# Performance work log

Hardware: AMD Instinct MI355X
Metric: run time of the kernel (lower is better)

The kernel has to match this reference:

```python
import jax, jax.numpy as jnp
import numpy as np

M = 30000      # total nodes
D = 64         # hidden_channels
B = 256        # number of graphs
E = 480000     # number of edges
NUM_ITER = 3   # Newton-Schulz iterations
EPS_TRIU = 0.001  # fix_triu diagonal jitter


def setup_inputs() -> dict:
    key = jax.random.key(0)
    k1, k2, k3 = jax.random.split(key, 3)
    x = jax.random.normal(k1, (M, D), dtype=jnp.float32)
    # sorted segment ids, every graph non-empty (sorted_randint semantics)
    batch = ((jnp.arange(M) * B) // M).astype(jnp.int32)
    edge = jax.random.randint(k2, (2, E), 0, M)
    W_att = jax.random.normal(k3, (D * D, 1), dtype=jnp.float32) / D
    b_att = jnp.zeros((1,), dtype=jnp.float32)
    return {"x": x, "batch": batch, "edge": edge, "W_att": W_att, "b_att": b_att}


def _segment_softmax(v, seg, num_segments):
    # v: [M], seg: [M] -> per-segment softmax
    m = jax.ops.segment_max(v, seg, num_segments=num_segments)
    e = jnp.exp(v - m[seg])
    s = jax.ops.segment_sum(e, seg, num_segments=num_segments)
    return e / s[seg]


def _sqrtm_ns(A, n_iter):
    # Newton-Schulz iterative matrix square root (MPN-COV Sqrtm)
    d = A.shape[-1]
    I = jnp.eye(d, dtype=A.dtype)
    normA = jnp.trace(A, axis1=-2, axis2=-1)[:, None, None]  # [B,1,1]
    Y = A / normA
    Z = jnp.broadcast_to(I, A.shape)
    for _ in range(n_iter):
        T = 0.5 * (3.0 * I - jnp.matmul(Z, Y))
        Y = jnp.matmul(Y, T)
        Z = jnp.matmul(T, Z)
    return Y * jnp.sqrt(normA)


def reference(x, batch, edge, W_att, b_att):
    Mn, Dd = x.shape
    # per-node outer products: einsum 'ik,kj->kij' on (x^T, x)
    wj = x[:, :, None] * x[:, None, :]              # [M, D, D]
    flat = wj.reshape(Mn, Dd * Dd)                  # [M, D*D]
    imp = (flat @ W_att + b_att)[:, 0]              # [M]
    imp = _segment_softmax(imp, batch, B)[:, None]  # scatter_softmax
    # scatter_mean(imp * flat, batch)
    num = jax.ops.segment_sum(imp * flat, batch, num_segments=B)
    cnt = jax.ops.segment_sum(jnp.ones((Mn,), x.dtype), batch, num_segments=B)
    out = (num / jnp.maximum(cnt, 1.0)[:, None]).reshape(B, Dd, Dd)
    # fix_triu: add eps * I before matrix sqrt
    out = out + EPS_TRIU * jnp.eye(Dd, dtype=out.dtype)
    out = _sqrtm_ns(out, NUM_ITER)
    # Triuvec: upper triangle incl. diagonal
    iu, ju = jnp.triu_indices(Dd)
    out = out[:, iu, ju]                            # [B, D*(D+1)/2]
    return out.reshape(B, -1)
```

## Files before the change

### kernel.cpp

```cpp
#include <hip/hip_runtime.h>
#include <math.h>

#define MN       30000
#define BSEG     256
#define EPS_TRIU 0.001f

#define XR_H 0
#define XR_L 8192
#define XT_H 16384
#define XT_L 24576
#define WT_H 32768
#define WT_L 36864
#define P_H 0
#define P_L 4096
#define Q_H 8192
#define Q_L 12288
#define R_H 16384
#define R_L 20480
#define S_H 24576
#define S_L 28672
#define V_H 32768
#define V_L 36864
#define IMP_F 20480
#define SWG_F 20608
#define SCL_F 20736
#define LDS_F4 5185

typedef __attribute__((ext_vector_type(8))) short bf16x8;
typedef __attribute__((ext_vector_type(4))) float f32x4;
#define MFMA_BF16(a, b, c) __builtin_amdgcn_mfma_f32_16x16x32_bf16(a, b, c, 0, 0, 0)

__device__ __forceinline__ short f2bf(float f) {
  unsigned u = __float_as_uint(f);
  u += 0x7FFF + ((u >> 16) & 1);
  return (short)(u >> 16);
}
__device__ __forceinline__ float bf2f(short s) {
  return __uint_as_float(((unsigned)(unsigned short)s) << 16);
}
__device__ __forceinline__ int sw64(int r, int c) { return (r << 6) + (c ^ ((r & 7) << 3)); }
__device__ __forceinline__ int sw128(int r, int c) { return (r << 7) + (c ^ ((r & 15) << 3)); }

template <int EPIT>
__device__ __forceinline__ void mm8(unsigned short* U, int dh, int dl,
                                    int ah_, int al_, int bh_, int bl_,
                                    int w, int r16, int kq) {
  const int mb = w >> 1;
  const int nb0 = (w & 1) << 1;
  const int ra = (mb << 4) + r16;
  const int mB = (mb << 4) + (kq << 2);
  bf16x8 Ah[2], Al[2];
#pragma unroll
  for (int ks = 0; ks < 2; ++ks) {
    const int ia = sw64(ra, (ks << 5) + (kq << 3));
    Ah[ks] = *(const bf16x8*)(U + ah_ + ia);
    Al[ks] = *(const bf16x8*)(U + al_ + ia);
  }
#pragma unroll
  for (int h = 0; h < 2; ++h) {
    const int nr = ((nb0 + h) << 4) + r16;
    bf16x8 Bh[2], Bl[2];
#pragma unroll
    for (int ks = 0; ks < 2; ++ks) {
      const int ib = sw64(nr, (ks << 5) + (kq << 3));
      Bh[ks] = *(const bf16x8*)(U + bh_ + ib);
      Bl[ks] = *(const bf16x8*)(U + bl_ + ib);
    }
    f32x4 acc = (f32x4)0.0f;
#pragma unroll
    for (int ks = 0; ks < 2; ++ks) {
      acc = MFMA_BF16(Ah[ks], Bh[ks], acc);
      acc = MFMA_BF16(Ah[ks], Bl[ks], acc);
      acc = MFMA_BF16(Al[ks], Bh[ks], acc);
    }
    short4 h4, l4;
#pragma unroll
    for (int e = 0; e < 4; ++e) {
      float v = acc[e];
      if (EPIT) v = -0.5f * v + ((mB + e) == nr ? 1.5f : 0.0f);
      const short hh = f2bf(v);
      ((short*)&h4)[e] = hh;
      ((short*)&l4)[e] = f2bf(v - bf2f(hh));
    }
    const int id = sw64(nr, mB);
    *(short4*)(U + dh + id) = h4;
    *(short4*)(U + dl + id) = l4;
  }
}

__device__ __forceinline__ void mm8_y3(unsigned short* U, int ah_, int al_,
                                       int bh_, int bl_, int w, float scale,
                                       float* __restrict__ ob, int r16, int kq) {
  const int mb = w >> 1;
  const int nb0 = (w & 1) << 1;
  if (mb > nb0 + 1) return;
  const int ra = (mb << 4) + r16;
  const int mB = (mb << 4) + (kq << 2);
  bf16x8 Ah[2], Al[2];
#pragma unroll
  for (int ks = 0; ks < 2; ++ks) {
    const int ia = sw64(ra, (ks << 5) + (kq << 3));
    Ah[ks] = *(const bf16x8*)(U + ah_ + ia);
    Al[ks] = *(const bf16x8*)(U + al_ + ia);
  }
#pragma unroll
  for (int h = 0; h < 2; ++h) {
    const int nb = nb0 + h;
    if (mb > nb) continue;
    const int nr = (nb << 4) + r16;
    bf16x8 Bh[2], Bl[2];
#pragma unroll
    for (int ks = 0; ks < 2; ++ks) {
      const int ib = sw64(nr, (ks << 5) + (kq << 3));
      Bh[ks] = *(const bf16x8*)(U + bh_ + ib);
      Bl[ks] = *(const bf16x8*)(U + bl_ + ib);
    }
    f32x4 acc = (f32x4)0.0f;
#pragma unroll
    for (int ks = 0; ks < 2; ++ks) {
      acc = MFMA_BF16(Ah[ks], Bh[ks], acc);
      acc = MFMA_BF16(Ah[ks], Bl[ks], acc);
      acc = MFMA_BF16(Al[ks], Bh[ks], acc);
    }
#pragma unroll
    for (int e = 0; e < 4; ++e) {
      const int m = mB + e;
      if (m <= nr) ob[((m * (129 - m)) >> 1) + nr - m] = acc[e] * scale;
    }
  }
}

template <int EPIT>
__device__ __forceinline__ void mm4(unsigned short* U, int dh, int dl,
                                    int ah_, int al_, int bh_, int bl_,
                                    int mq, int nq, int r16, int kq) {
  bf16x8 Ah[2][2], Al[2][2], Bh[2][2], Bl[2][2];
#pragma unroll
  for (int blk = 0; blk < 2; ++blk) {
    const int ra = (mq << 5) + (blk << 4) + r16;
    const int rb = (nq << 5) + (blk << 4) + r16;
#pragma unroll
    for (int ks = 0; ks < 2; ++ks) {
      const int co = (ks << 5) + (kq << 3);
      const int ia = sw64(ra, co), ib = sw64(rb, co);
      Ah[blk][ks] = *(const bf16x8*)(U + ah_ + ia);
      Al[blk][ks] = *(const bf16x8*)(U + al_ + ia);
      Bh[blk][ks] = *(const bf16x8*)(U + bh_ + ib);
      Bl[blk][ks] = *(const bf16x8*)(U + bl_ + ib);
    }
  }
#pragma unroll
  for (int mb = 0; mb < 2; ++mb)
#pragma unroll
    for (int nb = 0; nb < 2; ++nb) {
      f32x4 acc = (f32x4)0.0f;
#pragma unroll
      for (int ks = 0; ks < 2; ++ks) {
        acc = MFMA_BF16(Ah[mb][ks], Bh[nb][ks], acc);
        acc = MFMA_BF16(Ah[mb][ks], Bl[nb][ks], acc);
        acc = MFMA_BF16(Al[mb][ks], Bh[nb][ks], acc);
      }
      const int nr = (nq << 5) + (nb << 4) + r16;
      const int mB = (mq << 5) + (mb << 4) + (kq << 2);
      short4 h4, l4;
#pragma unroll
      for (int e = 0; e < 4; ++e) {
        float v = acc[e];
        if (EPIT) v = -0.5f * v + ((mB + e) == nr ? 1.5f : 0.0f);
        const short hh = f2bf(v);
        ((short*)&h4)[e] = hh;
        ((short*)&l4)[e] = f2bf(v - bf2f(hh));
      }
      const int id = sw64(nr, mB);
      *(short4*)(U + dh + id) = h4;
      *(short4*)(U + dl + id) = l4;
    }
}

extern "C" __global__ __launch_bounds__(512, 1) void readout_fused(
    const float* __restrict__ x, const float* __restrict__ Watt, float* __restrict__ out) {
  __shared__ float4 lds4[LDS_F4];
  float* ldsf = (float*)lds4;
  unsigned short* U = (unsigned short*)lds4;

  const int b = blockIdx.x;
  const int t = threadIdx.x;
  const int w = t >> 6, lane = t & 63;
  const int r16 = lane & 15, kq = lane >> 4;
  const int start = (b * MN + BSEG - 1) / BSEG;
  const int end = ((b + 1) * MN + BSEG - 1) / BSEG;
  const int n = end - start;

  const float4* W4 = (const float4*)Watt;
  const float4* X4 = (const float4*)x;

  if (t < 128) ldsf[IMP_F + t] = 0.0f;
  if (t == 128) ldsf[SCL_F] = 0.0f;
  const bool doW = (t < 256);
  const int kt = t >> 4, nt = t & 15;
  float4 gw[4];
  if (doW) {
#pragma unroll
    for (int i = 0; i < 4; ++i) gw[i] = W4[((kt << 2) + i) * 16 + nt];
  }
  {
    const int jt = t >> 4, dt = t & 15;
    const int j4 = jt << 2, d4 = dt << 2;
    float4 g[4];
#pragma unroll
    for (int i = 0; i < 4; ++i)
      g[i] = (j4 + i < n) ? X4[(size_t)(start + j4 + i) * 16 + dt]
                          : make_float4(0.f, 0.f, 0.f, 0.f);
    short hs[4][4], ls[4][4];
#pragma unroll
    for (int i = 0; i < 4; ++i)
#pragma unroll
      for (int e = 0; e < 4; ++e) {
        const float val = (&g[i].x)[e];
        const short hh = f2bf(val);
        hs[i][e] = hh;
        ls[i][e] = f2bf(val - bf2f(hh));
      }
#pragma unroll
    for (int i = 0; i < 4; ++i) {
      short4 h4, l4;
#pragma unroll
      for (int e = 0; e < 4; ++e) { ((short*)&h4)[e] = hs[i][e]; ((short*)&l4)[e] = ls[i][e]; }
      const int ir = sw64(j4 + i, d4);
      *(short4*)(U + XR_H + ir) = h4;
      *(short4*)(U + XR_L + ir) = l4;
    }
#pragma unroll
    for (int e = 0; e < 4; ++e) {
      short4 h4, l4;
#pragma unroll
      for (int i = 0; i < 4; ++i) { ((short*)&h4)[i] = hs[i][e]; ((short*)&l4)[i] = ls[i][e]; }
      const int it = sw128(d4 + e, j4);
      *(short4*)(U + XT_H + it) = h4;
      *(short4*)(U + XT_L + it) = l4;
    }
  }
  if (doW) {
    const int k4 = kt << 2, n4 = nt << 2;
#pragma unroll
    for (int e = 0; e < 4; ++e) {
      short4 h4, l4;
#pragma unroll
      for (int i = 0; i < 4; ++i) {
        const float val = (&gw[i].x)[e];
        const short hh = f2bf(val);
        ((short*)&h4)[i] = hh;
        ((short*)&l4)[i] = f2bf(val - bf2f(hh));
      }
      const int idx = sw64(n4 + e, k4);
      *(short4*)(U + WT_H + idx) = h4;
      *(short4*)(U + WT_L + idx) = l4;
    }
  }
  __syncthreads();

  {
    const int mq2 = w >> 1, nq2 = w & 1;
    bf16x8 Ah[2][2], Al[2][2];
#pragma unroll
    for (int mb = 0; mb < 2; ++mb) {
      const int ra = (mq2 << 5) + (mb << 4) + r16;
#pragma unroll
      for (int ks = 0; ks < 2; ++ks) {
        const int ia = sw64(ra, (ks << 5) + (kq << 3));
        Ah[mb][ks] = *(const bf16x8*)(U + XR_H + ia);
        Al[mb][ks] = *(const bf16x8*)(U + XR_L + ia);
      }
    }
    float c[2][4] = {};
#pragma unroll
    for (int nb = 0; nb < 2; ++nb) {
      const int rb = ((nq2 << 1) + nb) * 16 + r16;
      bf16x8 Bh[2], Bl[2];
#pragma unroll
      for (int ks = 0; ks < 2; ++ks) {
        const int ib = sw64(rb, (ks << 5) + (kq << 3));
        Bh[ks] = *(const bf16x8*)(U + WT_H + ib);
        Bl[ks] = *(const bf16x8*)(U + WT_L + ib);
      }
#pragma unroll
      for (int mb = 0; mb < 2; ++mb) {
        f32x4 acc = (f32x4)0.0f;
#pragma unroll
        for (int ks = 0; ks < 2; ++ks) {
          acc = MFMA_BF16(Ah[mb][ks], Bh[ks], acc);
          acc = MFMA_BF16(Ah[mb][ks], Bl[ks], acc);
          acc = MFMA_BF16(Al[mb][ks], Bh[ks], acc);
        }
        const int mBase = (mq2 << 5) + (mb << 4) + (kq << 2);
        const int xi = sw128(rb, mBase);
        short4 xh = *(const short4*)(U + XT_H + xi);
        short4 xl = *(const short4*)(U + XT_L + xi);
#pragma unroll
        for (int e = 0; e < 4; ++e)
          c[mb][e] += acc[e] * (bf2f(((short*)&xh)[e]) + bf2f(((short*)&xl)[e]));
      }
    }
#pragma unroll
    for (int s = 1; s <= 8; s <<= 1)
#pragma unroll
      for (int mb = 0; mb < 2; ++mb)
#pragma unroll
        for (int e = 0; e < 4; ++e) c[mb][e] += __shfl_xor(c[mb][e], s, 64);
    if (r16 == 0)
#pragma unroll
      for (int mb = 0; mb < 2; ++mb)
#pragma unroll
        for (int e = 0; e < 4; ++e)
          atomicAdd(&ldsf[IMP_F + (mq2 << 5) + (mb << 4) + (kq << 2) + e], c[mb][e]);
  }
  __syncthreads();

  bf16x8 pxh0 = *(const bf16x8*)(U + XT_H + t * 8);
  bf16x8 pxl0 = *(const bf16x8*)(U + XT_L + t * 8);
  bf16x8 pxh1 = *(const bf16x8*)(U + XT_H + (t + 512) * 8);
  bf16x8 pxl1 = *(const bf16x8*)(U + XT_L + (t + 512) * 8);
  if (t < 64) {
    float v0 = (t < n) ? ldsf[IMP_F + t] : -3.0e38f;
    float v1 = (t + 64 < n) ? ldsf[IMP_F + t + 64] : -3.0e38f;
    float m = fmaxf(v0, v1);
#pragma unroll
    for (int s = 32; s; s >>= 1) m = fmaxf(m, __shfl_xor(m, s, 64));
    float e0 = (t < n) ? expf(v0 - m) : 0.0f;
    float e1 = (t + 64 < n) ? expf(v1 - m) : 0.0f;
    float se = e0 + e1;
#pragma unroll
    for (int s = 32; s; s >>= 1) se += __shfl_xor(se, s, 64);
    const float inv = 1.0f / (se * (float)n);
    ldsf[SWG_F + t] = sqrtf(e0 * inv);
    ldsf[SWG_F + t + 64] = sqrtf(e1 * inv);
  }
  __syncthreads();

  {
    float ss = 0.0f;
#pragma unroll
    for (int g = 0; g < 2; ++g) {
      const int v = t + (g << 9);
      const int d = v >> 4;
      const int j0 = ((v & 15) << 3) ^ ((d & 15) << 3);
      bf16x8 hh = g ? pxh1 : pxh0;
      bf16x8 ll = g ? pxl1 : pxl0;
#pragma unroll
      for (int e = 0; e < 8; ++e) {
        const float val = (bf2f(hh[e]) + bf2f(ll[e])) * ldsf[SWG_F + j0 + e];
        ss = fmaf(val, val, ss);
        const short nh = f2bf(val);
        hh[e] = nh;
        ll[e] = f2bf(val - bf2f(nh));
      }
      *(bf16x8*)(U + XT_H + v * 8) = hh;
      *(bf16x8*)(U + XT_L + v * 8) = ll;
    }
#pragma unroll
    for (int s = 1; s <= 32; s <<= 1) ss += __shfl_xor(ss, s, 64);
    if (lane == 0) atomicAdd(&ldsf[SCL_F], ss);
  }
  __syncthreads();

  const float normA = ldsf[SCL_F] + 64.0f * EPS_TRIU;
  const float rn = 1.0f / normA;
  const float scale = sqrtf(normA);

  if (w < 4) {
    const int mq = w >> 1, nq = w & 1;
    bf16x8 Ah[2][4], Al[2][4];
#pragma unroll
    for (int mb = 0; mb < 2; ++mb) {
      const int ra = (mq << 5) + (mb << 4) + r16;
#pragma unroll
      for (int ks = 0; ks < 4; ++ks) {
        const int ia = sw128(ra, (ks << 5) + (kq << 3));
        Ah[mb][ks] = *(const bf16x8*)(U + XT_H + ia);
        Al[mb][ks] = *(const bf16x8*)(U + XT_L + ia);
      }
    }
#pragma unroll
    for (int nb = 0; nb < 2; ++nb) {
      const int nr = (nq << 5) + (nb << 4) + r16;
      bf16x8 Bh[4], Bl[4];
      if (mq == nq) {
#pragma unroll
        for (int ks = 0; ks < 4; ++ks) { Bh[ks] = Ah[nb][ks]; Bl[ks] = Al[nb][ks]; }
      } else {
#pragma unroll
        for (int ks = 0; ks < 4; ++ks) {
          const int ib = sw128(nr, (ks << 5) + (kq << 3));
          Bh[ks] = *(const bf16x8*)(U + XT_H + ib);
          Bl[ks] = *(const bf16x8*)(U + XT_L + ib);
        }
      }
#pragma unroll
      for (int mb = 0; mb < 2; ++mb) {
        f32x4 acc = (f32x4)0.0f;
#pragma unroll
        for (int ks = 0; ks < 4; ++ks) {
          acc = MFMA_BF16(Ah[mb][ks], Bh[ks], acc);
          acc = MFMA_BF16(Ah[mb][ks], Bl[ks], acc);
          acc = MFMA_BF16(Al[mb][ks], Bh[ks], acc);
        }
        const int mB = (mq << 5) + (mb << 4) + (kq << 2);
        short4 yh, yl, th, tl;
#pragma unroll
        for (int e = 0; e < 4; ++e) {
          const int diag = ((mB + e) == nr);
          const float a = acc[e] + (diag ? EPS_TRIU : 0.0f);
          const float y = a * rn;
          const short hh = f2bf(y);
          ((short*)&yh)[e] = hh;
          ((short*)&yl)[e] = f2bf(y - bf2f(hh));
          const float tv = (diag ? 1.5f : 0.0f) - 0.5f * y;
          const short th1 = f2bf(tv);
          ((short*)&th)[e] = th1;
          ((short*)&tl)[e] = f2bf(tv - bf2f(th1));
        }
        const int id = sw64(nr, mB);
        *(short4*)(U + P_H + id) = yh;
        *(short4*)(U + P_L + id) = yl;
        *(short4*)(U + V_H + id) = th;
        *(short4*)(U + V_L + id) = tl;
      }
    }
  }
  __syncthreads();

  mm8<0>(U, Q_H, Q_L, P_H, P_L, V_H, V_L, w, r16, kq);
  __syncthreads();
  mm8<1>(U, S_H, S_L, V_H, V_L, Q_H, Q_L, w, r16, kq);
  __syncthreads();
  if (w < 4)
    mm4<0>(U, R_H, R_L, Q_H, Q_L, S_H, S_L, w >> 1, w & 1, r16, kq);
  else
    mm4<0>(U, P_H, P_L, S_H, S_L, V_H, V_L, (w - 4) >> 1, (w - 4) & 1, r16, kq);
  __syncthreads();
  mm8<1>(U, V_H, V_L, P_H, P_L, R_H, R_L, w, r16, kq);
  __syncthreads();
  mm8_y3(U, R_H, R_L, V_H, V_L, w, scale, out + (size_t)b * 2080, r16, kq);
}

extern "C" void kernel_launch(void* const* d_in, const int* in_sizes, int n_in,
                              void* d_out, int out_size, void* d_ws, size_t ws_size,
                              hipStream_t stream) {
  const float* x = (const float*)d_in[0];
  const float* Watt = (const float*)d_in[3];
  float* out = (float*)d_out;
  readout_fused<<<dim3(BSEG), dim3(512), 0, stream>>>(x, Watt, out);
}
```

Measured before the change: 16.89 us.

## Use truncating bf16 split and restructure importance matmul to avoid atomics

Replaces round-to-nearest bf16 conversion with a truncation-based hi/lo split, which takes fewer ALU ops per element, and applies it everywhere. The importance-score computation is reorganized so each wave owns 16 node rows and loops over all four output column blocks. It then reduces within the wave by shuffles and writes results directly, removing the LDS atomics and the zero-initialisation. Truncation slightly changes the precision of the hi part, but the lo term compensates.

```diff
diff --git a/kernel.cpp b/kernel.cpp
--- a/kernel.cpp
+++ b/kernel.cpp
@@ -30,13 +30,14 @@
 typedef __attribute__((ext_vector_type(4))) float f32x4;
 #define MFMA_BF16(a, b, c) __builtin_amdgcn_mfma_f32_16x16x32_bf16(a, b, c, 0, 0, 0)
 
-__device__ __forceinline__ short f2bf(float f) {
-  unsigned u = __float_as_uint(f);
-  u += 0x7FFF + ((u >> 16) & 1);
-  return (short)(u >> 16);
-}
 __device__ __forceinline__ float bf2f(short s) {
   return __uint_as_float(((unsigned)(unsigned short)s) << 16);
+}
+__device__ __forceinline__ void split2(float val, unsigned short& h, unsigned short& l) {
+  const unsigned u = __float_as_uint(val);
+  h = (unsigned short)(u >> 16);
+  const float lo = val - __uint_as_float(u & 0xFFFF0000u);
+  l = (unsigned short)(__float_as_uint(lo) >> 16);
 }
 __device__ __forceinline__ int sw64(int r, int c) { return (r << 6) + (c ^ ((r & 7) << 3)); }
 __device__ __forceinline__ int sw128(int r, int c) { return (r << 7) + (c ^ ((r & 15) << 3)); }
@@ -78,9 +79,10 @@
     for (int e = 0; e < 4; ++e) {
       float v = acc[e];
       if (EPIT) v = -0.5f * v + ((mB + e) == nr ? 1.5f : 0.0f);
-      const short hh = f2bf(v);
-      ((short*)&h4)[e] = hh;
-      ((short*)&l4)[e] = f2bf(v - bf2f(hh));
+      unsigned short hh, ll;
+      split2(v, hh, ll);
+      ((unsigned short*)&h4)[e] = hh;
+      ((unsigned short*)&l4)[e] = ll;
     }
     const int id = sw64(nr, mB);
     *(short4*)(U + dh + id) = h4;
@@ -167,9 +169,10 @@
       for (int e = 0; e < 4; ++e) {
         float v = acc[e];
         if (EPIT) v = -0.5f * v + ((mB + e) == nr ? 1.5f : 0.0f);
-        const short hh = f2bf(v);
-        ((short*)&h4)[e] = hh;
-        ((short*)&l4)[e] = f2bf(v - bf2f(hh));
+        unsigned short hh, ll;
+        split2(v, hh, ll);
+        ((unsigned short*)&h4)[e] = hh;
+        ((unsigned short*)&l4)[e] = ll;
       }
       const int id = sw64(nr, mB);
       *(short4*)(U + dh + id) = h4;
@@ -194,8 +197,7 @@
   const float4* W4 = (const float4*)Watt;
   const float4* X4 = (const float4*)x;
 
-  if (t < 128) ldsf[IMP_F + t] = 0.0f;
-  if (t == 128) ldsf[SCL_F] = 0.0f;
+  if (t == 0) ldsf[SCL_F] = 0.0f;
   const bool doW = (t < 256);
   const int kt = t >> 4, nt = t & 15;
   float4 gw[4];
@@ -211,21 +213,19 @@
     for (int i = 0; i < 4; ++i)
       g[i] = (j4 + i < n) ? X4[(size_t)(start + j4 + i) * 16 + dt]
                           : make_float4(0.f, 0.f, 0.f, 0.f);
-    short hs[4][4], ls[4][4];
+    unsigned short hs[4][4], ls[4][4];
 #pragma unroll
     for (int i = 0; i < 4; ++i)
 #pragma unroll
-      for (int e = 0; e < 4; ++e) {
-        const float val = (&g[i].x)[e];
-        const short hh = f2bf(val);
-        hs[i][e] = hh;
-        ls[i][e] = f2bf(val - bf2f(hh));
-      }
+      for (int e = 0; e < 4; ++e) split2((&g[i].x)[e], hs[i][e], ls[i][e]);
 #pragma unroll
     for (int i = 0; i < 4; ++i) {
       short4 h4, l4;
 #pragma unroll
-      for (int e = 0; e < 4; ++e) { ((short*)&h4)[e] = hs[i][e]; ((short*)&l4)[e] = ls[i][e]; }
+      for (int e = 0; e < 4; ++e) {
+        ((unsigned short*)&h4)[e] = hs[i][e];
+        ((unsigned short*)&l4)[e] = ls[i][e];
+      }
       const int ir = sw64(j4 + i, d4);
       *(short4*)(U + XR_H + ir) = h4;
       *(short4*)(U + XR_L + ir) = l4;
@@ -234,7 +234,10 @@
     for (int e = 0; e < 4; ++e) {
       short4 h4, l4;
 #pragma unroll
-      for (int i = 0; i < 4; ++i) { ((short*)&h4)[i] = hs[i][e]; ((short*)&l4)[i] = ls[i][e]; }
+      for (int i = 0; i < 4; ++i) {
+        ((unsigned short*)&h4)[i] = hs[i][e];
+        ((unsigned short*)&l4)[i] = ls[i][e];
+      }
       const int it = sw128(d4 + e, j4);
       *(short4*)(U + XT_H + it) = h4;
       *(short4*)(U + XT_L + it) = l4;
@@ -247,10 +250,10 @@
       short4 h4, l4;
 #pragma unroll
       for (int i = 0; i < 4; ++i) {
-        const float val = (&gw[i].x)[e];
-        const short hh = f2bf(val);
-        ((short*)&h4)[i] = hh;
-        ((short*)&l4)[i] = f2bf(val - bf2f(hh));
+        unsigned short hh, ll;
+        split2((&gw[i].x)[e], hh, ll);
+        ((unsigned short*)&h4)[i] = hh;
+        ((unsigned short*)&l4)[i] = ll;
       }
       const int idx = sw64(n4 + e, k4);
       *(short4*)(U + WT_H + idx) = h4;
@@ -260,59 +263,41 @@
   __syncthreads();
 
   {
-    const int mq2 = w >> 1, nq2 = w & 1;
-    bf16x8 Ah[2][2], Al[2][2];
-#pragma unroll
-    for (int mb = 0; mb < 2; ++mb) {
-      const int ra = (mq2 << 5) + (mb << 4) + r16;
+    const int jrow = (w << 4) + r16;
+    bf16x8 Bh[2], Bl[2];
+#pragma unroll
+    for (int ks = 0; ks < 2; ++ks) {
+      const int ib = sw64(jrow, (ks << 5) + (kq << 3));
+      Bh[ks] = *(const bf16x8*)(U + XR_H + ib);
+      Bl[ks] = *(const bf16x8*)(U + XR_L + ib);
+    }
+    float partial = 0.0f;
+#pragma unroll
+    for (int mb = 0; mb < 4; ++mb) {
+      bf16x8 Ah[2], Al[2];
 #pragma unroll
       for (int ks = 0; ks < 2; ++ks) {
-        const int ia = sw64(ra, (ks << 5) + (kq << 3));
-        Ah[mb][ks] = *(const bf16x8*)(U + XR_H + ia);
-        Al[mb][ks] = *(const bf16x8*)(U + XR_L + ia);
-      }
-    }
-    float c[2][4] = {};
-#pragma unroll
-    for (int nb = 0; nb < 2; ++nb) {
-      const int rb = ((nq2 << 1) + nb) * 16 + r16;
-      bf16x8 Bh[2], Bl[2];
+        const int ia = sw64((mb << 4) + r16, (ks << 5) + (kq << 3));
+        Ah[ks] = *(const bf16x8*)(U + WT_H + ia);
+        Al[ks] = *(const bf16x8*)(U + WT_L + ia);
+      }
+      f32x4 acc = (f32x4)0.0f;
 #pragma unroll
       for (int ks = 0; ks < 2; ++ks) {
-        const int ib = sw64(rb, (ks << 5) + (kq << 3));
-        Bh[ks] = *(const bf16x8*)(U + WT_H + ib);
-        Bl[ks] = *(const bf16x8*)(U + WT_L + ib);
-      }
-#pragma unroll
-      for (int mb = 0; mb < 2; ++mb) {
-        f32x4 acc = (f32x4)0.0f;
-#pragma unroll
-        for (int ks = 0; ks < 2; ++ks) {
-          acc = MFMA_BF16(Ah[mb][ks], Bh[ks], acc);
-          acc = MFMA_BF16(Ah[mb][ks], Bl[ks], acc);
-          acc = MFMA_BF16(Al[mb][ks], Bh[ks], acc);
-        }
-        const int mBase = (mq2 << 5) + (mb << 4) + (kq << 2);
-        const int xi = sw128(rb, mBase);
-        short4 xh = *(const short4*)(U + XT_H + xi);
-        short4 xl = *(const short4*)(U + XT_L + xi);
-#pragma unroll
-        for (int e = 0; e < 4; ++e)
-          c[mb][e] += acc[e] * (bf2f(((short*)&xh)[e]) + bf2f(((short*)&xl)[e]));
-      }
-    }
-#pragma unroll
-    for (int s = 1; s <= 8; s <<= 1)
-#pragma unroll
-      for (int mb = 0; mb < 2; ++mb)
-#pragma unroll
-        for (int e = 0; e < 4; ++e) c[mb][e] += __shfl_xor(c[mb][e], s, 64);
-    if (r16 == 0)
-#pragma unroll
-      for (int mb = 0; mb < 2; ++mb)
-#pragma unroll
-        for (int e = 0; e < 4; ++e)
-          atomicAdd(&ldsf[IMP_F + (mq2 << 5) + (mb << 4) + (kq << 2) + e], c[mb][e]);
+        acc = MFMA_BF16(Ah[ks], Bh[ks], acc);
+        acc = MFMA_BF16(Ah[ks], Bl[ks], acc);
+        acc = MFMA_BF16(Al[ks], Bh[ks], acc);
+      }
+      const int xi = sw64(jrow, (mb << 4) + (kq << 2));
+      const short4 xh = *(const short4*)(U + XR_H + xi);
+      const short4 xl = *(const short4*)(U + XR_L + xi);
+#pragma unroll
+      for (int e = 0; e < 4; ++e)
+        partial += acc[e] * (bf2f(((const short*)&xh)[e]) + bf2f(((const short*)&xl)[e]));
+    }
+    partial += __shfl_xor(partial, 16, 64);
+    partial += __shfl_xor(partial, 32, 64);
+    if (kq == 0) ldsf[IMP_F + jrow] = partial;
   }
   __syncthreads();
 
@@ -350,9 +335,10 @@
       for (int e = 0; e < 8; ++e) {
         const float val = (bf2f(hh[e]) + bf2f(ll[e])) * ldsf[SWG_F + j0 + e];
         ss = fmaf(val, val, ss);
-        const short nh = f2bf(val);
-        hh[e] = nh;
-        ll[e] = f2bf(val - bf2f(nh));
+        unsigned short nh, nl;
+        split2(val, nh, nl);
+        hh[e] = (short)nh;
+        ll[e] = (short)nl;
       }
       *(bf16x8*)(U + XT_H + v * 8) = hh;
       *(bf16x8*)(U + XT_L + v * 8) = ll;
@@ -411,13 +397,14 @@
           const int diag = ((mB + e) == nr);
           const float a = acc[e] + (diag ? EPS_TRIU : 0.0f);
           const float y = a * rn;
-          const short hh = f2bf(y);
-          ((short*)&yh)[e] = hh;
-          ((short*)&yl)[e] = f2bf(y - bf2f(hh));
+          unsigned short hh, ll;
+          split2(y, hh, ll);
+          ((unsigned short*)&yh)[e] = hh;
+          ((unsigned short*)&yl)[e] = ll;
           const float tv = (diag ? 1.5f : 0.0f) - 0.5f * y;
-          const short th1 = f2bf(tv);
-          ((short*)&th)[e] = th1;
-          ((short*)&tl)[e] = f2bf(tv - bf2f(th1));
+          split2(tv, hh, ll);
+          ((unsigned short*)&th)[e] = hh;
+          ((unsigned short*)&tl)[e] = ll;
         }
         const int id = sw64(nr, mB);
         *(short4*)(U + P_H + id) = yh;
```

After: 14.98 us. -11.3%, faster.
